# Optimization experiments

Measured on AMD Instinct MI355X. Metric: run time of the kernel, lower is better.

Reference implementation:

```python
import jax, jax.numpy as jnp
import numpy as np

B, S, I, H, O, L = 256, 512, 256, 256, 256, 64


def setup_inputs() -> dict:
    key = jax.random.key(0)
    ks = jax.random.split(key, 12)
    def lin(k, fan_in, fan_out):
        kw, kb = jax.random.split(k)
        lim = 1.0 / np.sqrt(fan_in)
        W = jax.random.uniform(kw, (fan_in, fan_out), jnp.float32, -lim, lim)
        b = jax.random.uniform(kb, (fan_out,), jnp.float32, -lim, lim)
        return W, b
    x = jax.random.normal(ks[0], (B, S, I), jnp.float32)
    W1x, b1x = lin(ks[1], I, H)   # rnn1.Wax
    W1a, b1a = lin(ks[2], H, H)   # rnn1.Waa
    W2x, b2x = lin(ks[3], O, H)   # rnn2.Wax
    W2a, b2a = lin(ks[4], H, H)   # rnn2.Waa
    Wy, by = lin(ks[5], H, O)     # Wya
    return {"x": x, "W1x": W1x, "b1x": b1x, "W1a": W1a, "b1a": b1a,
            "W2x": W2x, "b2x": b2x, "W2a": W2a, "b2a": b2a, "Wy": Wy, "by": by}


def reference(x, W1x, b1x, W1a, b1a, W2x, b2x, W2a, b2a, Wy, by):
    batch = x.shape[0]
    a0 = jnp.zeros((batch, W1a.shape[0]), x.dtype)  # a[:, -1] is zeros at encoder start

    # Encoder: a_t = tanh(Wax(x_t) + Waa(a_{t-1}))
    def enc_step(a, x_t):
        a = jnp.tanh(x_t @ W1x + b1x + a @ W1a + b1a)
        return a, None
    a_last, _ = jax.lax.scan(enc_step, a0, jnp.swapaxes(x, 0, 1))  # [S,B,I] scan

    # Torch code: y_pred[:,0] set from encoder, then decoder reads y_pred[:,i]
    # BEFORE overwriting it -> input is y0 at i=0, zeros for i>0.
    y0 = jax.nn.sigmoid(a_last @ Wy + by)  # [B,O]
    zero_in = jnp.zeros_like(y0)

    def dec_step(a, i):
        inp = jnp.where(i == 0, y0, zero_in)
        a = jnp.tanh(inp @ W2x + b2x + a @ W2a + b2a)
        y = jax.nn.sigmoid(a @ Wy + by)
        return a, y
    _, ys = jax.lax.scan(dec_step, a_last, jnp.arange(L))  # ys: [L,B,O]
    return jnp.swapaxes(ys, 0, 1)  # [B,L,O]
```

## Files before the change

### kernel.cpp

```cpp
#include <hip/hip_runtime.h>

typedef unsigned short u16;
typedef unsigned int   u32;
typedef __attribute__((ext_vector_type(8))) __bf16 bf16x8;
typedef __attribute__((ext_vector_type(8))) u16    u16x8;
typedef __attribute__((ext_vector_type(4))) float  f32x4;
typedef __attribute__((ext_vector_type(4))) u32    u32x4;
typedef __attribute__((ext_vector_type(2))) u32    u32x2;

#define MFMA16(a,b,c) __builtin_amdgcn_mfma_f32_16x16x32_bf16((a),(b),(c),0,0,0)
#define C_TANH 2.8853900817779268f
#define NL2E  -1.4426950408889634f

__device__ __forceinline__ float ubit(u32 x){ return __builtin_bit_cast(float, x); }
__device__ __forceinline__ u16 f2b(float f){
    u32 b = __builtin_bit_cast(u32, f);
    b += 0x7FFFu + ((b >> 16) & 1u);
    return (u16)(b >> 16);
}
__device__ __forceinline__ u32 pkbf(float a, float b){ return ((u32)f2b(b) << 16) | (u32)f2b(a); }
__device__ __forceinline__ u32 pk_away(float a, float b){
    u32 ua = (__builtin_bit_cast(u32, a) + 0x8000u) >> 16;
    u32 ub = (__builtin_bit_cast(u32, b) + 0x8000u) & 0xFFFF0000u;
    return ub | ua;
}
__device__ __forceinline__ void bar_lds(){ __asm__ volatile("s_waitcnt lgkmcnt(0)\n\ts_barrier" ::: "memory"); }

__global__ __launch_bounds__(256, 1) void k1_xw(const float* __restrict__ x, const float* __restrict__ w1x,
                                               const float* __restrict__ b1x, const float* __restrict__ b1a,
                                               u16* __restrict__ xpre)
{
    const int t = blockIdx.x;
    const int tid = threadIdx.x, lane = tid & 63, w = tid >> 6;
    const int l15 = lane & 15, q = lane >> 4;
    const int lrow = l15 & 7, hi = l15 >> 3;
    const int cw = w * 64;

    bf16x8 bw[4][8];
    f32x4 biasv[4];
    #pragma unroll
    for (int nt = 0; nt < 4; ++nt){
        const int n0 = cw + nt * 16 + q * 4;
        f32x4 bx = *(const f32x4*)(b1x + n0);
        f32x4 ba = *(const f32x4*)(b1a + n0);
        biasv[nt] = (bx + ba) * C_TANH;
        const int n = cw + nt * 16 + l15;
        #pragma unroll
        for (int ks = 0; ks < 8; ++ks){
            u16x8 tt;
            #pragma unroll
            for (int j = 0; j < 8; ++j) tt[j] = f2b(w1x[(ks * 32 + q * 8 + j) * 256 + n] * C_TANH);
            bw[nt][ks] = __builtin_bit_cast(bf16x8, tt);
        }
    }

    for (int blk = 0; blk < 16; ++blk){
        const int b0r = blk * 16;
        bf16x8 av[8];
        #pragma unroll
        for (int ks = 0; ks < 8; ++ks){
            const float* p = x + ((size_t)(b0r + l15) * 512 + t) * 256 + ks * 32 + q * 8;
            f32x4 v0 = *(const f32x4*)p;
            f32x4 v1 = *(const f32x4*)(p + 4);
            u32x4 dd = { pkbf(v0[0], v0[1]), pkbf(v0[2], v0[3]),
                         pkbf(v1[0], v1[1]), pkbf(v1[2], v1[3]) };
            av[ks] = __builtin_bit_cast(bf16x8, dd);
        }
        f32x4 acc[4];
        #pragma unroll
        for (int nt = 0; nt < 4; ++nt) acc[nt] = biasv[nt];
        #pragma unroll
        for (int ks = 0; ks < 8; ++ks)
            #pragma unroll
            for (int nt = 0; nt < 4; ++nt)
                acc[nt] = MFMA16(bw[nt][ks], av[ks], acc[nt]);
        const int bg = blk * 2 + hi;
        #pragma unroll
        for (int p2 = 0; p2 < 2; ++p2){
            const int w8 = w * 2 + p2;
            const size_t a16 = ((((size_t)t * 32 + bg) * 8 + w8) * 32 + q * 8 + lrow) * 8;
            u32x4 V = { pkbf(acc[p2 * 2][0], acc[p2 * 2][1]), pkbf(acc[p2 * 2][2], acc[p2 * 2][3]),
                        pkbf(acc[p2 * 2 + 1][0], acc[p2 * 2 + 1][1]), pkbf(acc[p2 * 2 + 1][2], acc[p2 * 2 + 1][3]) };
            *(u32x4*)(xpre + a16) = V;
        }
    }
}

__global__ __launch_bounds__(512, 2) void k2_enc(const float* __restrict__ w1a, const u16* __restrict__ xpre,
                                                u16* __restrict__ alast)
{
    __shared__ __align__(16) u16 st[2][8][264];
    const int tid = threadIdx.x, lane = tid & 63, w = tid >> 6;
    const int l15 = lane & 15, q = lane >> 4;
    const int lrow = l15 & 7, hi = l15 >> 3;
    const int bg = blockIdx.x;

    bf16x8 bw[2][8];
    #pragma unroll
    for (int nt = 0; nt < 2; ++nt){
        const int n = w * 32 + nt * 16 + l15;
        #pragma unroll
        for (int ks = 0; ks < 8; ++ks){
            u16x8 tt;
            #pragma unroll
            for (int j = 0; j < 8; ++j) tt[j] = f2b(w1a[(ks * 32 + q * 8 + j) * 256 + n] * C_TANH);
            bw[nt][ks] = __builtin_bit_cast(bf16x8, tt);
        }
    }
    for (int i = tid; i < 8 * 264; i += 512) (&st[0][0][0])[i] = 0;
    __syncthreads();

    const u16* xp = xpre + ((((size_t)bg) * 8 + w) * 32 + q * 8 + lrow) * 8;
    u32x4 c = *(const u32x4*)xp;
    u32x4 a = *(const u32x4*)(xp + 65536);

    const u16 (*sR)[264] = st[0];
    u16 (*sW)[264] = st[1];

    for (int t = 0; t < 512; ++t){
        const size_t tp = (size_t)((t + 2 < 512) ? t + 2 : 511) * 65536;
        u32x4 n_ = *(const u32x4*)(xp + tp);

        bf16x8 av[8];
        #pragma unroll
        for (int ks = 0; ks < 8; ++ks)
            av[ks] = *(const bf16x8*)&sR[lrow][ks * 32 + q * 8];

        f32x4 acc[2];
        #pragma unroll
        for (int nt = 0; nt < 2; ++nt)
            #pragma unroll
            for (int r = 0; r < 4; ++r){
                const u32 d = c[nt * 2 + (r >> 1)];
                acc[nt][r] = ubit((r & 1) ? (d & 0xFFFF0000u) : (d << 16));
            }
        #pragma unroll
        for (int ks = 0; ks < 8; ++ks)
            #pragma unroll
            for (int nt = 0; nt < 2; ++nt)
                acc[nt] = MFMA16(bw[nt][ks], av[ks], acc[nt]);

        float m[4];
        #pragma unroll
        for (int r = 0; r < 4; ++r){
            const float mv = hi ? acc[1][r] : acc[0][r];
            const float e = __builtin_amdgcn_exp2f(mv);
            m[r] = 1.0f - 2.0f * __builtin_amdgcn_rcpf(e + 1.0f);
        }
        u32x2 hp = { pk_away(m[0], m[1]), pk_away(m[2], m[3]) };
        *(u32x2*)&sW[lrow][w * 32 + hi * 16 + q * 4] = hp;

        c = a; a = n_;
        bar_lds();
        const u16 (*tmp)[264] = sR; sR = (const u16(*)[264])sW; sW = (u16(*)[264])tmp;
    }
    if (tid < 256){
        const int row = tid >> 5, c8 = (tid & 31) * 8;
        *(u32x4*)(alast + (size_t)(bg * 8 + row) * 256 + c8) = *(const u32x4*)&sR[row][c8];
    }
}

__global__ __launch_bounds__(256, 1) void k3_pre(const float* __restrict__ wy, const float* __restrict__ by,
                                                const float* __restrict__ w2x,
                                                const u16* __restrict__ alast, float* __restrict__ injws)
{
    __shared__ __align__(16) u16 st[16][264];
    __shared__ __align__(16) u16 y0s[16][264];
    const int tid = threadIdx.x, lane = tid & 63, w = tid >> 6;
    const int l15 = lane & 15, q = lane >> 4;
    const int lrow = l15 & 7, hi = l15 >> 3;
    const int bg = blockIdx.x;
    {
        const int row = tid >> 4, c = (tid & 15) * 16;
        #pragma unroll
        for (int j = 0; j < 2; ++j)
            *(u32x4*)&st[row][c + j * 8] = *(const u32x4*)(alast + (size_t)(bg * 16 + row) * 256 + c + j * 8);
    }
    __syncthreads();
    {
        bf16x8 bwy[4][8];
        f32x4 biasy[4];
        #pragma unroll
        for (int nt = 0; nt < 4; ++nt){
            const int n0 = w * 64 + nt * 16 + q * 4;
            biasy[nt] = (*(const f32x4*)(by + n0)) * NL2E;
            const int n = w * 64 + nt * 16 + l15;
            #pragma unroll
            for (int ks = 0; ks < 8; ++ks){
                u16x8 tt;
                #pragma unroll
                for (int j = 0; j < 8; ++j) tt[j] = f2b(wy[(ks * 32 + q * 8 + j) * 256 + n] * NL2E);
                bwy[nt][ks] = __builtin_bit_cast(bf16x8, tt);
            }
        }
        bf16x8 av[8];
        #pragma unroll
        for (int ks = 0; ks < 8; ++ks) av[ks] = *(const bf16x8*)&st[l15][ks * 32 + q * 8];
        f32x4 acc[4];
        #pragma unroll
        for (int nt = 0; nt < 4; ++nt) acc[nt] = biasy[nt];
        #pragma unroll
        for (int ks = 0; ks < 8; ++ks)
            #pragma unroll
            for (int nt = 0; nt < 4; ++nt) acc[nt] = MFMA16(bwy[nt][ks], av[ks], acc[nt]);
        #pragma unroll
        for (int nt = 0; nt < 4; ++nt){
            float y[4];
            #pragma unroll
            for (int r = 0; r < 4; ++r) y[r] = __builtin_amdgcn_rcpf(1.0f + __builtin_amdgcn_exp2f(acc[nt][r]));
            u32x2 hp = { pkbf(y[0], y[1]), pkbf(y[2], y[3]) };
            *(u32x2*)&y0s[l15][w * 64 + nt * 16 + q * 4] = hp;
        }
    }
    __syncthreads();
    {
        bf16x8 av[8];
        #pragma unroll
        for (int ks = 0; ks < 8; ++ks) av[ks] = *(const bf16x8*)&y0s[l15][ks * 32 + q * 8];
        f32x4 acc[4];
        #pragma unroll
        for (int nt = 0; nt < 4; ++nt) acc[nt] = (f32x4){0.f, 0.f, 0.f, 0.f};
        #pragma unroll
        for (int ks = 0; ks < 8; ++ks)
            #pragma unroll
            for (int nt = 0; nt < 4; ++nt){
                const int n = w * 64 + nt * 16 + l15;
                u16x8 tt;
                #pragma unroll
                for (int j = 0; j < 8; ++j) tt[j] = f2b(w2x[(ks * 32 + q * 8 + j) * 256 + n] * C_TANH);
                acc[nt] = MFMA16(__builtin_bit_cast(bf16x8, tt), av[ks], acc[nt]);
            }
        #pragma unroll
        for (int nt = 0; nt < 4; ++nt){
            const size_t ib = ((((size_t)(bg * 2 + hi)) * 8 + (size_t)(w * 2 + (nt >> 1))) * 32
                               + q * 8 + lrow) * 8 + (nt & 1) * 4;
            *(f32x4*)(injws + ib) = acc[nt];
        }
    }
}

__global__ __launch_bounds__(512, 2) void k3_rec(const float* __restrict__ w2a, const float* __restrict__ b2x,
                                                const float* __restrict__ b2a, const u16* __restrict__ alast,
                                                const float* __restrict__ injws, u16* __restrict__ astate)
{
    __shared__ __align__(16) u16 st[2][8][264];
    const int tid = threadIdx.x, lane = tid & 63, w = tid >> 6;
    const int l15 = lane & 15, q = lane >> 4;
    const int lrow = l15 & 7, hi = l15 >> 3;
    const int bg = blockIdx.x;

    bf16x8 bw[2][8];
    f32x4 bias2[2];
    #pragma unroll
    for (int nt = 0; nt < 2; ++nt){
        const int n0 = w * 32 + nt * 16 + q * 4;
        f32x4 bx = *(const f32x4*)(b2x + n0);
        f32x4 ba = *(const f32x4*)(b2a + n0);
        bias2[nt] = (bx + ba) * C_TANH;
        const int n = w * 32 + nt * 16 + l15;
        #pragma unroll
        for (int ks = 0; ks < 8; ++ks){
            u16x8 tt;
            #pragma unroll
            for (int j = 0; j < 8; ++j) tt[j] = f2b(w2a[(ks * 32 + q * 8 + j) * 256 + n] * C_TANH);
            bw[nt][ks] = __builtin_bit_cast(bf16x8, tt);
        }
    }
    f32x4 ini[2];
    {
        const size_t ib = (((size_t)bg * 8 + w) * 32 + q * 8 + lrow) * 8;
        #pragma unroll
        for (int nt = 0; nt < 2; ++nt)
            ini[nt] = *(const f32x4*)(injws + ib + nt * 4) + bias2[nt];
    }
    if (tid < 256){
        const int row = tid >> 5, c8 = (tid & 31) * 8;
        *(u32x4*)&st[0][row][c8] = *(const u32x4*)(alast + (size_t)(bg * 8 + row) * 256 + c8);
    }
    __syncthreads();

    const u16 (*sR)[264] = st[0];
    u16 (*sW)[264] = st[1];

    for (int i = 0; i < 64; ++i){
        bf16x8 av[8];
        #pragma unroll
        for (int ks = 0; ks < 8; ++ks) av[ks] = *(const bf16x8*)&sR[lrow][ks * 32 + q * 8];
        f32x4 acc[2];
        #pragma unroll
        for (int nt = 0; nt < 2; ++nt) acc[nt] = ini[nt];
        #pragma unroll
        for (int ks = 0; ks < 8; ++ks)
            #pragma unroll
            for (int nt = 0; nt < 2; ++nt) acc[nt] = MFMA16(bw[nt][ks], av[ks], acc[nt]);

        float m[4];
        #pragma unroll
        for (int r = 0; r < 4; ++r){
            const float mv = hi ? acc[1][r] : acc[0][r];
            const float e = __builtin_amdgcn_exp2f(mv);
            m[r] = 1.0f - 2.0f * __builtin_amdgcn_rcpf(e + 1.0f);
        }
        u32x2 hp = { pk_away(m[0], m[1]), pk_away(m[2], m[3]) };
        *(u32x2*)&sW[lrow][w * 32 + hi * 16 + q * 4] = hp;
        *(u32x2*)(astate + ((size_t)i * 256 + bg * 8 + lrow) * 256
                          + w * 32 + hi * 16 + q * 4) = hp;

        if (i == 0){
            #pragma unroll
            for (int nt = 0; nt < 2; ++nt) ini[nt] = bias2[nt];
        }
        bar_lds();
        const u16 (*tmp)[264] = sR; sR = (const u16(*)[264])sW; sW = (u16(*)[264])tmp;
    }
}

__global__ __launch_bounds__(256, 1) void k3_out(const float* __restrict__ wy, const float* __restrict__ by,
                                                const u16* __restrict__ astate, float* __restrict__ out)
{
    const int tid = threadIdx.x, lane = tid & 63, w = tid >> 6;
    const int l15 = lane & 15, q = lane >> 4;

    bf16x8 bwy[4][8];
    f32x4 biasy[4];
    #pragma unroll
    for (int nt = 0; nt < 4; ++nt){
        const int n0 = w * 64 + nt * 16 + q * 4;
        biasy[nt] = (*(const f32x4*)(by + n0)) * NL2E;
        const int n = w * 64 + nt * 16 + l15;
        #pragma unroll
        for (int ks = 0; ks < 8; ++ks){
            u16x8 tt;
            #pragma unroll
            for (int j = 0; j < 8; ++j) tt[j] = f2b(wy[(ks * 32 + q * 8 + j) * 256 + n] * NL2E);
            bwy[nt][ks] = __builtin_bit_cast(bf16x8, tt);
        }
    }
    #pragma unroll
    for (int tix = 0; tix < 4; ++tix){
        const int R0 = (blockIdx.x * 4 + tix) * 16;
        bf16x8 av[8];
        #pragma unroll
        for (int ks = 0; ks < 8; ++ks)
            av[ks] = *(const bf16x8*)(astate + (size_t)(R0 + l15) * 256 + ks * 32 + q * 8);
        f32x4 acc[4];
        #pragma unroll
        for (int nt = 0; nt < 4; ++nt) acc[nt] = biasy[nt];
        #pragma unroll
        for (int ks = 0; ks < 8; ++ks)
            #pragma unroll
            for (int nt = 0; nt < 4; ++nt) acc[nt] = MFMA16(bwy[nt][ks], av[ks], acc[nt]);
        const int R = R0 + l15, ii = R >> 8, b = R & 255;
        #pragma unroll
        for (int nt = 0; nt < 4; ++nt){
            f32x4 o4;
            #pragma unroll
            for (int r = 0; r < 4; ++r)
                o4[r] = __builtin_amdgcn_rcpf(1.0f + __builtin_amdgcn_exp2f(acc[nt][r]));
            *(f32x4*)(out + ((size_t)b * 64 + ii) * 256 + w * 64 + nt * 16 + q * 4) = o4;
        }
    }
}

extern "C" void kernel_launch(void* const* d_in, const int* in_sizes, int n_in,
                              void* d_out, int out_size, void* d_ws, size_t ws_size,
                              hipStream_t stream) {
    const float* x   = (const float*)d_in[0];
    const float* w1x = (const float*)d_in[1];
    const float* b1x = (const float*)d_in[2];
    const float* w1a = (const float*)d_in[3];
    const float* b1a = (const float*)d_in[4];
    const float* w2x = (const float*)d_in[5];
    const float* b2x = (const float*)d_in[6];
    const float* w2a = (const float*)d_in[7];
    const float* b2a = (const float*)d_in[8];
    const float* wy  = (const float*)d_in[9];
    const float* by  = (const float*)d_in[10];

    u16*   xpre   = (u16*)d_ws;
    u16*   astate = (u16*)d_ws;
    u16*   alast  = xpre + (size_t)512 * 16 * 512 * 8;
    float* injws  = (float*)(alast + 256 * 256);
    float* o      = (float*)d_out;

    k1_xw <<<512, 256, 0, stream>>>(x, w1x, b1x, b1a, xpre);
    k2_enc<<<32,  512, 0, stream>>>(w1a, xpre, alast);
    k3_pre<<<16,  256, 0, stream>>>(wy, by, w2x, alast, injws);
    k3_rec<<<32,  512, 0, stream>>>(w2a, b2x, b2a, alast, injws, astate);
    k3_out<<<256, 256, 0, stream>>>(wy, by, astate, o);
}
```

Measured before the change: 585.4 us.

## Split recurrent kernels into 4-row batch groups across 64 blocks

Cuts the batch rows per workgroup in the encoder and decoder recurrence kernels from 8 to 4 and doubles the grid from 32 to 64 blocks. The precomputed-input layout in k1_xw and k3_pre is changed to match. Each lane now handles 2 tanh outputs instead of 4, which shortens the per-step critical path of the serial loop and puts more CUs to work. The cost is that MFMA tiles are only partly used (4 of 16 columns useful), the weights are loaded redundantly by twice as many blocks, and the LDS row stride is repadded to 272.

```diff
diff --git a/kernel.cpp b/kernel.cpp
--- a/kernel.cpp
+++ b/kernel.cpp
@@ -33,7 +33,6 @@
     const int t = blockIdx.x;
     const int tid = threadIdx.x, lane = tid & 63, w = tid >> 6;
     const int l15 = lane & 15, q = lane >> 4;
-    const int lrow = l15 & 7, hi = l15 >> 3;
     const int cw = w * 64;
 
     bf16x8 bw[4][8];
@@ -74,11 +73,10 @@
             #pragma unroll
             for (int nt = 0; nt < 4; ++nt)
                 acc[nt] = MFMA16(bw[nt][ks], av[ks], acc[nt]);
-        const int bg = blk * 2 + hi;
+        const int bg = blk * 4 + (l15 >> 2), b4 = l15 & 3;
         #pragma unroll
         for (int p2 = 0; p2 < 2; ++p2){
-            const int w8 = w * 2 + p2;
-            const size_t a16 = ((((size_t)t * 32 + bg) * 8 + w8) * 32 + q * 8 + lrow) * 8;
+            const size_t a16 = ((((size_t)t * 64 + bg) * 8 + (w * 2 + p2)) * 16 + q * 4 + b4) * 8;
             u32x4 V = { pkbf(acc[p2 * 2][0], acc[p2 * 2][1]), pkbf(acc[p2 * 2][2], acc[p2 * 2][3]),
                         pkbf(acc[p2 * 2 + 1][0], acc[p2 * 2 + 1][1]), pkbf(acc[p2 * 2 + 1][2], acc[p2 * 2 + 1][3]) };
             *(u32x4*)(xpre + a16) = V;
@@ -89,10 +87,12 @@
 __global__ __launch_bounds__(512, 2) void k2_enc(const float* __restrict__ w1a, const u16* __restrict__ xpre,
                                                 u16* __restrict__ alast)
 {
-    __shared__ __align__(16) u16 st[2][8][264];
-    const int tid = threadIdx.x, lane = tid & 63, w = tid >> 6;
-    const int l15 = lane & 15, q = lane >> 4;
-    const int lrow = l15 & 7, hi = l15 >> 3;
+    __shared__ __align__(16) u16 st[2][4][272];
+    const int tid = threadIdx.x, lane = tid & 63, w = tid >> 6;
+    const int l15 = lane & 15, q = lane >> 4;
+    const int b4 = l15 & 3;
+    const bool selnt = (l15 & 4) != 0, selrp = (l15 & 8) != 0;
+    const int wcol = w * 32 + (selnt ? 16 : 0) + q * 4 + (selrp ? 2 : 0);
     const int bg = blockIdx.x;
 
     bf16x8 bw[2][8];
@@ -107,15 +107,15 @@
             bw[nt][ks] = __builtin_bit_cast(bf16x8, tt);
         }
     }
-    for (int i = tid; i < 8 * 264; i += 512) (&st[0][0][0])[i] = 0;
+    for (int i = tid; i < 4 * 272; i += 512) (&st[0][0][0])[i] = 0;
     __syncthreads();
 
-    const u16* xp = xpre + ((((size_t)bg) * 8 + w) * 32 + q * 8 + lrow) * 8;
+    const u16* xp = xpre + (((size_t)bg * 8 + w) * 16 + q * 4 + b4) * 8;
     u32x4 c = *(const u32x4*)xp;
     u32x4 a = *(const u32x4*)(xp + 65536);
 
-    const u16 (*sR)[264] = st[0];
-    u16 (*sW)[264] = st[1];
+    const u16 (*sR)[272] = st[0];
+    u16 (*sW)[272] = st[1];
 
     for (int t = 0; t < 512; ++t){
         const size_t tp = (size_t)((t + 2 < 512) ? t + 2 : 511) * 65536;
@@ -124,7 +124,7 @@
         bf16x8 av[8];
         #pragma unroll
         for (int ks = 0; ks < 8; ++ks)
-            av[ks] = *(const bf16x8*)&sR[lrow][ks * 32 + q * 8];
+            av[ks] = *(const bf16x8*)&sR[b4][ks * 32 + q * 8];
 
         f32x4 acc[2];
         #pragma unroll
@@ -140,23 +140,25 @@
             for (int nt = 0; nt < 2; ++nt)
                 acc[nt] = MFMA16(bw[nt][ks], av[ks], acc[nt]);
 
-        float m[4];
-        #pragma unroll
-        for (int r = 0; r < 4; ++r){
-            const float mv = hi ? acc[1][r] : acc[0][r];
-            const float e = __builtin_amdgcn_exp2f(mv);
-            m[r] = 1.0f - 2.0f * __builtin_amdgcn_rcpf(e + 1.0f);
-        }
-        u32x2 hp = { pk_away(m[0], m[1]), pk_away(m[2], m[3]) };
-        *(u32x2*)&sW[lrow][w * 32 + hi * 16 + q * 4] = hp;
+        const float s0 = selnt ? acc[1][0] : acc[0][0];
+        const float s1 = selnt ? acc[1][1] : acc[0][1];
+        const float s2 = selnt ? acc[1][2] : acc[0][2];
+        const float s3 = selnt ? acc[1][3] : acc[0][3];
+        const float mv0 = selrp ? s2 : s0;
+        const float mv1 = selrp ? s3 : s1;
+        const float e0 = __builtin_amdgcn_exp2f(mv0);
+        const float t0 = 1.0f - 2.0f * __builtin_amdgcn_rcpf(e0 + 1.0f);
+        const float e1 = __builtin_amdgcn_exp2f(mv1);
+        const float t1 = 1.0f - 2.0f * __builtin_amdgcn_rcpf(e1 + 1.0f);
+        *(u32*)&sW[b4][wcol] = pk_away(t0, t1);
 
         c = a; a = n_;
         bar_lds();
-        const u16 (*tmp)[264] = sR; sR = (const u16(*)[264])sW; sW = (u16(*)[264])tmp;
-    }
-    if (tid < 256){
+        const u16 (*tmp)[272] = sR; sR = (const u16(*)[272])sW; sW = (u16(*)[272])tmp;
+    }
+    if (tid < 128){
         const int row = tid >> 5, c8 = (tid & 31) * 8;
-        *(u32x4*)(alast + (size_t)(bg * 8 + row) * 256 + c8) = *(const u32x4*)&sR[row][c8];
+        *(u32x4*)(alast + (size_t)(bg * 4 + row) * 256 + c8) = *(const u32x4*)&sR[row][c8];
     }
 }
 
@@ -168,7 +170,6 @@
     __shared__ __align__(16) u16 y0s[16][264];
     const int tid = threadIdx.x, lane = tid & 63, w = tid >> 6;
     const int l15 = lane & 15, q = lane >> 4;
-    const int lrow = l15 & 7, hi = l15 >> 3;
     const int bg = blockIdx.x;
     {
         const int row = tid >> 4, c = (tid & 15) * 16;
@@ -230,11 +231,12 @@
                 for (int j = 0; j < 8; ++j) tt[j] = f2b(w2x[(ks * 32 + q * 8 + j) * 256 + n] * C_TANH);
                 acc[nt] = MFMA16(__builtin_bit_cast(bf16x8, tt), av[ks], acc[nt]);
             }
-        #pragma unroll
-        for (int nt = 0; nt < 4; ++nt){
-            const size_t ib = ((((size_t)(bg * 2 + hi)) * 8 + (size_t)(w * 2 + (nt >> 1))) * 32
-                               + q * 8 + lrow) * 8 + (nt & 1) * 4;
-            *(f32x4*)(injws + ib) = acc[nt];
+        const int bgr = bg * 4 + (l15 >> 2), b4 = l15 & 3;
+        #pragma unroll
+        for (int p2 = 0; p2 < 2; ++p2){
+            const size_t ib = (((size_t)bgr * 8 + (size_t)(w * 2 + p2)) * 16 + q * 4 + b4) * 8;
+            *(f32x4*)(injws + ib)     = acc[p2 * 2];
+            *(f32x4*)(injws + ib + 4) = acc[p2 * 2 + 1];
         }
     }
 }
@@ -243,10 +245,12 @@
                                                 const float* __restrict__ b2a, const u16* __restrict__ alast,
                                                 const float* __restrict__ injws, u16* __restrict__ astate)
 {
-    __shared__ __align__(16) u16 st[2][8][264];
-    const int tid = threadIdx.x, lane = tid & 63, w = tid >> 6;
-    const int l15 = lane & 15, q = lane >> 4;
-    const int lrow = l15 & 7, hi = l15 >> 3;
+    __shared__ __align__(16) u16 st[2][4][272];
+    const int tid = threadIdx.x, lane = tid & 63, w = tid >> 6;
+    const int l15 = lane & 15, q = lane >> 4;
+    const int b4 = l15 & 3;
+    const bool selnt = (l15 & 4) != 0, selrp = (l15 & 8) != 0;
+    const int wcol = w * 32 + (selnt ? 16 : 0) + q * 4 + (selrp ? 2 : 0);
     const int bg = blockIdx.x;
 
     bf16x8 bw[2][8];
@@ -268,24 +272,24 @@
     }
     f32x4 ini[2];
     {
-        const size_t ib = (((size_t)bg * 8 + w) * 32 + q * 8 + lrow) * 8;
+        const size_t ib = (((size_t)bg * 8 + w) * 16 + q * 4 + b4) * 8;
         #pragma unroll
         for (int nt = 0; nt < 2; ++nt)
             ini[nt] = *(const f32x4*)(injws + ib + nt * 4) + bias2[nt];
     }
-    if (tid < 256){
+    if (tid < 128){
         const int row = tid >> 5, c8 = (tid & 31) * 8;
-        *(u32x4*)&st[0][row][c8] = *(const u32x4*)(alast + (size_t)(bg * 8 + row) * 256 + c8);
+        *(u32x4*)&st[0][row][c8] = *(const u32x4*)(alast + (size_t)(bg * 4 + row) * 256 + c8);
     }
     __syncthreads();
 
-    const u16 (*sR)[264] = st[0];
-    u16 (*sW)[264] = st[1];
+    const u16 (*sR)[272] = st[0];
+    u16 (*sW)[272] = st[1];
 
     for (int i = 0; i < 64; ++i){
         bf16x8 av[8];
         #pragma unroll
-        for (int ks = 0; ks < 8; ++ks) av[ks] = *(const bf16x8*)&sR[lrow][ks * 32 + q * 8];
+        for (int ks = 0; ks < 8; ++ks) av[ks] = *(const bf16x8*)&sR[b4][ks * 32 + q * 8];
         f32x4 acc[2];
         #pragma unroll
         for (int nt = 0; nt < 2; ++nt) acc[nt] = ini[nt];
@@ -294,24 +298,26 @@
             #pragma unroll
             for (int nt = 0; nt < 2; ++nt) acc[nt] = MFMA16(bw[nt][ks], av[ks], acc[nt]);
 
-        float m[4];
-        #pragma unroll
-        for (int r = 0; r < 4; ++r){
-            const float mv = hi ? acc[1][r] : acc[0][r];
-            const float e = __builtin_amdgcn_exp2f(mv);
-            m[r] = 1.0f - 2.0f * __builtin_amdgcn_rcpf(e + 1.0f);
-        }
-        u32x2 hp = { pk_away(m[0], m[1]), pk_away(m[2], m[3]) };
-        *(u32x2*)&sW[lrow][w * 32 + hi * 16 + q * 4] = hp;
-        *(u32x2*)(astate + ((size_t)i * 256 + bg * 8 + lrow) * 256
-                          + w * 32 + hi * 16 + q * 4) = hp;
+        const float s0 = selnt ? acc[1][0] : acc[0][0];
+        const float s1 = selnt ? acc[1][1] : acc[0][1];
+        const float s2 = selnt ? acc[1][2] : acc[0][2];
+        const float s3 = selnt ? acc[1][3] : acc[0][3];
+        const float mv0 = selrp ? s2 : s0;
+        const float mv1 = selrp ? s3 : s1;
+        const float e0 = __builtin_amdgcn_exp2f(mv0);
+        const float t0 = 1.0f - 2.0f * __builtin_amdgcn_rcpf(e0 + 1.0f);
+        const float e1 = __builtin_amdgcn_exp2f(mv1);
+        const float t1 = 1.0f - 2.0f * __builtin_amdgcn_rcpf(e1 + 1.0f);
+        const u32 hp = pk_away(t0, t1);
+        *(u32*)&sW[b4][wcol] = hp;
+        *(u32*)(astate + ((size_t)i * 256 + bg * 4 + b4) * 256 + wcol) = hp;
 
         if (i == 0){
             #pragma unroll
             for (int nt = 0; nt < 2; ++nt) ini[nt] = bias2[nt];
         }
         bar_lds();
-        const u16 (*tmp)[264] = sR; sR = (const u16(*)[264])sW; sW = (u16(*)[264])tmp;
+        const u16 (*tmp)[272] = sR; sR = (const u16(*)[272])sW; sW = (u16(*)[272])tmp;
     }
 }
 
@@ -384,8 +390,8 @@
     float* o      = (float*)d_out;
 
     k1_xw <<<512, 256, 0, stream>>>(x, w1x, b1x, b1a, xpre);
-    k2_enc<<<32,  512, 0, stream>>>(w1a, xpre, alast);
+    k2_enc<<<64,  512, 0, stream>>>(w1a, xpre, alast);
     k3_pre<<<16,  256, 0, stream>>>(wy, by, w2x, alast, injws);
-    k3_rec<<<32,  512, 0, stream>>>(w2a, b2x, b2a, alast, injws, astate);
+    k3_rec<<<64,  512, 0, stream>>>(w2a, b2x, b2a, alast, injws, astate);
     k3_out<<<256, 256, 0, stream>>>(wy, by, astate, o);
 }
```

Result: faster. 555.1 us (-5.2%).
